# Kernel tuning notes

Measured on AMD Instinct MI355X. Metric: run time of the kernel, lower is better.

## Reference

```python
import jax, jax.numpy as jnp
import numpy as np

EMBED = 1024
HEAD = 64


def setup_inputs() -> dict:
    key = jax.random.key(0)
    kx, kq, kk, kv = jax.random.split(key, 4)
    x = jax.random.normal(kx, (8, 2048, EMBED), dtype=jnp.float32)
    s = EMBED ** -0.5  # init scale for weights
    Wq = jax.random.normal(kq, (EMBED, HEAD), dtype=jnp.float32) * s
    Wk = jax.random.normal(kk, (EMBED, HEAD), dtype=jnp.float32) * s
    Wv = jax.random.normal(kv, (EMBED, HEAD), dtype=jnp.float32) * s
    return {"x": x, "Wq": Wq, "Wk": Wk, "Wv": Wv}


def reference(x, Wq, Wk, Wv):
    # x: [B, T, C]; single-head causal attention, scale = C**-0.5 (embed dim, as in source)
    B, T, C = x.shape
    q = jnp.einsum('btc,ch->bth', x, Wq)
    k = jnp.einsum('btc,ch->bth', x, Wk)
    v = jnp.einsum('btc,ch->bth', x, Wv)
    w = jnp.einsum('bqh,bkh->bqk', q, k) * (C ** -0.5)  # [B, T, T]
    causal = jnp.tril(jnp.ones((T, T), dtype=bool))
    w = jnp.where(causal, w, -jnp.inf)
    w = jax.nn.softmax(w, axis=-1)
    # dropout = 0.0 (eval-mode reference) -> identity
    return jnp.einsum('bqk,bkh->bqh', w, v)  # [B, T, head]
```

## Files before the change

kernel.cpp:

```cpp
#include <hip/hip_runtime.h>
#include <stdint.h>

typedef unsigned short u16;
typedef __attribute__((ext_vector_type(8))) short short8;
typedef __attribute__((ext_vector_type(4))) float f32x4;
typedef __attribute__((ext_vector_type(16))) float f32x16;

#define B_ 8
#define T_ 2048
#define C_ 1024
#define D_ 64
#define PSC 0.04508422f

__device__ inline uint32_t pack2(float lo, float hi) {
  uint32_t r;
  asm("v_cvt_pk_bf16_f32 %0, %1, %2" : "=v"(r) : "v"(lo), "v"(hi));
  return r;
}
__device__ inline u16 f2bf(float f) {
  uint32_t r;
  asm("v_cvt_pk_bf16_f32 %0, %1, %2" : "=v"(r) : "v"(f), "v"(f));
  return (u16)r;
}

__global__ __launch_bounds__(256) void wt_kernel(const float* __restrict__ Wq,
                                                 const float* __restrict__ Wk,
                                                 const float* __restrict__ Wv,
                                                 u16* __restrict__ wfrag) {
  const int mi = blockIdx.x >> 4;
  const int k0 = (blockIdx.x & 15) * 64;
  const float* W = (mi == 0) ? Wq : ((mi == 1) ? Wk : Wv);
  const float sc = (mi == 0) ? PSC : 1.0f;
  __shared__ u16 tr[64 * 68];

  const int t = threadIdx.x;
  {
    const int n = t & 63, kr0 = (t >> 6) * 16;
#pragma unroll
    for (int j = 0; j < 16; ++j)
      tr[n * 68 + kr0 + j] = f2bf(W[(size_t)(k0 + kr0 + j) * 64 + n] * sc);
  }
  __syncthreads();
  {
    const int n = t >> 2, q16 = (t & 3) * 16;
    const int n16g = mi * 4 + (n >> 4);
#pragma unroll
    for (int h = 0; h < 2; ++h) {
      const int kr = q16 + h * 8;
      const int kchunk = (k0 + kr) >> 5;
      const int lane = (n & 15) + 16 * ((kr >> 3) & 3);
      uint32_t pk[4];
#pragma unroll
      for (int jj = 0; jj < 4; ++jj)
        pk[jj] = (uint32_t)tr[n * 68 + kr + 2 * jj] | ((uint32_t)tr[n * 68 + kr + 2 * jj + 1] << 16);
      *(uint4*)&wfrag[(((size_t)n16g * 32 + kchunk) * 64 + lane) * 8] = *(uint4*)&pk[0];
    }
  }
}

__global__ __launch_bounds__(512, 1) void qkv_kernel(const float* __restrict__ x,
                                                     const u16* __restrict__ wfrag,
                                                     u16* __restrict__ qfr,
                                                     u16* __restrict__ kfr,
                                                     u16* __restrict__ vfr) {
  __shared__ __align__(16) u16 xl[2][64 * 64];

  const int tid = threadIdx.x;
  const int w = tid >> 6, l = tid & 63;
  const int lo16 = l & 15, hi4 = l >> 4;
  const int wh = w & 1, ng = w >> 1;
  const int m0 = blockIdx.x * 64;

  const int xrow = tid >> 3;
  const int xc8 = tid & 7;
  const float* xs0 = x + (size_t)(m0 + xrow) * C_ + xc8 * 8;
  u16* xdst0 = &xl[0][xrow * 64 + ((xc8 ^ (xrow & 7)) << 3)];
  u16* xdst1 = &xl[1][xrow * 64 + ((xc8 ^ (xrow & 7)) << 3)];

  f32x4 acc[2][3];
#pragma unroll
  for (int rf = 0; rf < 2; ++rf)
#pragma unroll
    for (int j = 0; j < 3; ++j) acc[rf][j] = {0.f, 0.f, 0.f, 0.f};

  const u16* wbase = wfrag + (size_t)(ng * 3) * 32 * 512 + l * 8;
  short8 wA[6], wB[6];
  float4 xr1a, xr1b, xr2a, xr2b;

#define LOADW(DST, KT)                                                        \
  _Pragma("unroll")                                                           \
  for (int i = 0; i < 6; ++i)                                                 \
    DST[i] = *(const short8*)(wbase + ((i >> 1) * 32 + (KT) * 2 + (i & 1)) * 512);

#define PACKX(A0, A1, DST)                                                    \
  { uint32_t p[4] = {pack2(A0.x, A0.y), pack2(A0.z, A0.w),                    \
                     pack2(A1.x, A1.y), pack2(A1.z, A1.w)};                   \
    *(uint4*)DST = *(uint4*)&p[0]; }

#define MFMA6(XR, WC)                                                         \
  _Pragma("unroll")                                                           \
  for (int k32 = 0; k32 < 2; ++k32) {                                         \
    const int ac = k32 * 4 + hi4;                                             \
    _Pragma("unroll")                                                         \
    for (int rf = 0; rf < 2; ++rf) {                                          \
      const int arow = wh * 32 + rf * 16 + lo16;                              \
      short8 a = *(const short8*)&XR[arow * 64 + ((ac ^ (arow & 7)) << 3)];   \
      _Pragma("unroll")                                                       \
      for (int j = 0; j < 3; ++j)                                             \
        acc[rf][j] = __builtin_amdgcn_mfma_f32_16x16x32_bf16(a, WC[j * 2 + k32], acc[rf][j], 0, 0, 0); \
    }                                                                         \
  }

  {
    float4 f0 = *(const float4*)(xs0 + 0);
    float4 f1 = *(const float4*)(xs0 + 4);
    PACKX(f0, f1, xdst0)
    xr1a = *(const float4*)(xs0 + 64);
    xr1b = *(const float4*)(xs0 + 68);
    LOADW(wA, 0)
  }
  __syncthreads();

#pragma unroll 1
  for (int kt = 0; kt < 14; kt += 2) {
    xr2a = *(const float4*)(xs0 + (kt + 2) * 64);
    xr2b = *(const float4*)(xs0 + (kt + 2) * 64 + 4);
    LOADW(wB, kt + 1)
    MFMA6(xl[0], wA)
    PACKX(xr1a, xr1b, xdst1)
    __syncthreads();
    xr1a = *(const float4*)(xs0 + (kt + 3) * 64);
    xr1b = *(const float4*)(xs0 + (kt + 3) * 64 + 4);
    LOADW(wA, kt + 2)
    MFMA6(xl[1], wB)
    PACKX(xr2a, xr2b, xdst0)
    __syncthreads();
  }
  LOADW(wB, 15)
  MFMA6(xl[0], wA)
  PACKX(xr1a, xr1b, xdst1)
  __syncthreads();
  MFMA6(xl[1], wB)
#undef LOADW
#undef PACKX
#undef MFMA6

  const int bb = m0 >> 11;
  const int tok_b = m0 & 2047;
#pragma unroll
  for (int rf = 0; rf < 2; ++rf) {
    const int row0 = wh * 32 + rf * 16 + hi4 * 4;
    const int tok0 = tok_b + row0;
    const int tt = tok0 >> 6;
    const int t32 = tok0 >> 5;
#pragma unroll
    for (int j = 0; j < 3; ++j) {
      const int cb = ng * 48 + j * 16;
      const int mt = cb >> 6;
      const int col = (cb & 63) + lo16;
      if (mt == 0) {
        const int cs = col >> 4;
        const int lane0 = (tok0 & 31) + 32 * ((col >> 3) & 1);
        u16* qp = qfr + ((((size_t)bb * 64 + t32) * 4 + cs) * 64 + lane0) * 8 + (col & 7);
#pragma unroll
        for (int r = 0; r < 4; ++r) qp[(size_t)r * 8] = f2bf(acc[rf][j][r]);
      } else if (mt == 1) {
        const int h = (tok0 >> 5) & 1;
        const int cs = col >> 4;
        const int lane0 = (tok0 & 31) + 32 * ((col >> 3) & 1);
        u16* kp = kfr + (((((size_t)bb * 32 + tt) * 2 + h) * 4 + cs) * 64 + lane0) * 8 + (col & 7);
#pragma unroll
        for (int r = 0; r < 4; ++r) kp[(size_t)r * 8] = f2bf(acc[rf][j][r]);
      } else {
        const int ks = (tok0 >> 4) & 3;
        const int hi = (tok0 >> 3) & 1;
        const int jj = tok0 & 7;
        const int lane = (col & 31) + 32 * hi;
        const int df = col >> 5;
        uint2 st = {pack2(acc[rf][j][0], acc[rf][j][1]), pack2(acc[rf][j][2], acc[rf][j][3])};
        *(uint2*)&vfr[((((((size_t)bb * 32 + tt) * 4 + ks) * 2 + df) * 64 + lane) * 8 + jj)] = st;
      }
    }
  }
}

__global__ __launch_bounds__(256, 2) void attn_kernel(const u16* __restrict__ qfr,
                                                      const u16* __restrict__ kfr,
                                                      const u16* __restrict__ vfr,
                                                      float* __restrict__ out) {
  __shared__ float o_lds[4][32][68];
  __shared__ float l_lds[4][64];

  const int tid = threadIdx.x;
  const int w = tid >> 6, l = tid & 63;
  const int l31 = l & 31, hi1 = l >> 5;
  const int b = blockIdx.x;
  const int y = blockIdx.y;
  const int qt = (y < 32) ? (63 - 2 * y) : (2 * (y - 32));
  const int qbase = qt * 32;
  const int boff = b * T_;
  const int NT = (qt + 2) >> 1;

  short8 qf[4];
  {
    const u16* qp = qfr + (size_t)(b * 64 + qt) * 4 * 512 + l * 8;
#pragma unroll
    for (int cs = 0; cs < 4; ++cs) qf[cs] = *(const short8*)(qp + cs * 512);
  }

  const u16* kfb = kfr + (size_t)b * 32 * 4096 + l * 8;
  const u16* vfb = vfr + (size_t)b * 32 * 4096 + l * 8;

  f32x16 O0, O1;
#pragma unroll
  for (int r = 0; r < 16; ++r) { O0[r] = 0.f; O1[r] = 0.f; }
  float lsum = 0.f;

  short8 kf[2][4];
#define LOADK(T) { const u16* kp = kfb + (size_t)(T) * 4096; \
  _Pragma("unroll") for (int h2 = 0; h2 < 2; ++h2) \
  _Pragma("unroll") for (int cs = 0; cs < 4; ++cs) \
    kf[h2][cs] = *(const short8*)(kp + (h2 * 4 + cs) * 512); }

  if (w < NT) LOADK(w);

  union { uint32_t u[4]; short8 v; } pu;
  short8 pa[4];

#pragma unroll 1
  for (int t = w; t < NT; t += 4) {
    const int k0 = t * 64;

    short8 vf[4][2];
    {
      const u16* vp = vfb + (size_t)t * 4096;
#pragma unroll
      for (int ks = 0; ks < 4; ++ks)
#pragma unroll
        for (int df = 0; df < 2; ++df)
          vf[ks][df] = *(const short8*)(vp + (ks * 2 + df) * 512);
    }

    f32x16 s0, s1, s0b, s1b;
#pragma unroll
    for (int r = 0; r < 16; ++r) { s0[r] = 0.f; s1[r] = 0.f; s0b[r] = 0.f; s1b[r] = 0.f; }
    __builtin_amdgcn_s_setprio(1);
#pragma unroll
    for (int cs = 0; cs < 2; ++cs) {
      s0 = __builtin_amdgcn_mfma_f32_32x32x16_bf16(kf[0][cs], qf[cs], s0, 0, 0, 0);
      s1 = __builtin_amdgcn_mfma_f32_32x32x16_bf16(kf[1][cs], qf[cs], s1, 0, 0, 0);
      s0b = __builtin_amdgcn_mfma_f32_32x32x16_bf16(kf[0][cs + 2], qf[cs + 2], s0b, 0, 0, 0);
      s1b = __builtin_amdgcn_mfma_f32_32x32x16_bf16(kf[1][cs + 2], qf[cs + 2], s1b, 0, 0, 0);
    }
    __builtin_amdgcn_s_setprio(0);
#pragma unroll
    for (int r = 0; r < 16; ++r) { s0[r] += s0b[r]; s1[r] += s1b[r]; }

    if (t + 4 < NT) LOADK(t + 4);

    if (k0 + 63 > qbase) {
#pragma unroll
      for (int r = 0; r < 16; ++r) {
        const int kr = (r & 3) + 8 * (r >> 2) + 4 * hi1;
        if (k0 + kr > qbase + l31) s0[r] = -1e30f;
        if (k0 + 32 + kr > qbase + l31) s1[r] = -1e30f;
      }
    }

    float p0[16], p1[16];
    float ts[4] = {0.f, 0.f, 0.f, 0.f};
#pragma unroll
    for (int r = 0; r < 16; ++r) {
      p0[r] = exp2f(s0[r]);
      p1[r] = exp2f(s1[r]);
      ts[r & 3] += p0[r] + p1[r];
    }
    lsum += (ts[0] + ts[1]) + (ts[2] + ts[3]);

#define REDIST(KS, ARR) { \
    const int s8 = ((KS) & 1) * 8; \
    uint32_t c0a = pack2(ARR[s8 + 0], ARR[s8 + 1]); \
    uint32_t c0b = pack2(ARR[s8 + 2], ARR[s8 + 3]); \
    uint32_t c1a = pack2(ARR[s8 + 4], ARR[s8 + 5]); \
    uint32_t c1b = pack2(ARR[s8 + 6], ARR[s8 + 7]); \
    uint32_t fa = hi1 ? c0a : c1a; \
    uint32_t fb = hi1 ? c0b : c1b; \
    uint32_t ga = __shfl_xor(fa, 32); \
    uint32_t gb = __shfl_xor(fb, 32); \
    pu.u[0] = hi1 ? ga : c0a; \
    pu.u[1] = hi1 ? gb : c0b; \
    pu.u[2] = hi1 ? c1a : ga; \
    pu.u[3] = hi1 ? c1b : gb; \
    pa[KS] = pu.v; }
    REDIST(0, p0)
    REDIST(1, p0)
    REDIST(2, p1)
    REDIST(3, p1)
#undef REDIST

    __builtin_amdgcn_s_setprio(1);
#pragma unroll
    for (int ks = 0; ks < 4; ++ks) {
      O0 = __builtin_amdgcn_mfma_f32_32x32x16_bf16(pa[ks], vf[ks][0], O0, 0, 0, 0);
      O1 = __builtin_amdgcn_mfma_f32_32x32x16_bf16(pa[ks], vf[ks][1], O1, 0, 0, 0);
    }
    __builtin_amdgcn_s_setprio(0);
  }
#undef LOADK

#pragma unroll
  for (int r = 0; r < 16; ++r) {
    const int qr = (r & 3) + 8 * (r >> 2) + 4 * hi1;
    o_lds[w][qr][l31] = O0[r];
    o_lds[w][qr][32 + l31] = O1[r];
  }
  l_lds[w][l] = lsum;
  __syncthreads();

  {
    const int q = tid >> 3;
    const int d8 = (tid & 7) * 8;
    float lacc = 0.f;
    float oacc[8] = {0.f, 0.f, 0.f, 0.f, 0.f, 0.f, 0.f, 0.f};
#pragma unroll
    for (int s = 0; s < 4; ++s) {
      lacc += l_lds[s][q] + l_lds[s][q + 32];
#pragma unroll
      for (int j = 0; j < 8; ++j) oacc[j] += o_lds[s][q][d8 + j];
    }
    const float inv = 1.f / lacc;
    float4 r0 = {oacc[0] * inv, oacc[1] * inv, oacc[2] * inv, oacc[3] * inv};
    float4 r1 = {oacc[4] * inv, oacc[5] * inv, oacc[6] * inv, oacc[7] * inv};
    float* op = out + (size_t)(boff + qbase + q) * 64 + d8;
    *(float4*)(op + 0) = r0;
    *(float4*)(op + 4) = r1;
  }
}

extern "C" void kernel_launch(void* const* d_in, const int* in_sizes, int n_in,
                              void* d_out, int out_size, void* d_ws, size_t ws_size,
                              hipStream_t stream) {
  const float* x  = (const float*)d_in[0];
  const float* Wq = (const float*)d_in[1];
  const float* Wk = (const float*)d_in[2];
  const float* Wv = (const float*)d_in[3];
  float* out = (float*)d_out;

  u16* ws    = (u16*)d_ws;
  u16* wfrag = ws;
  u16* qfr   = ws + 196608;
  u16* kfr   = qfr + 1048576;
  u16* vfr   = kfr + 1048576;

  wt_kernel<<<dim3(48), dim3(256), 0, stream>>>(Wq, Wk, Wv, wfrag);
  qkv_kernel<<<dim3(256), dim3(512), 0, stream>>>(x, wfrag, qfr, kfr, vfr);
  attn_kernel<<<dim3(8, 64), dim3(256), 0, stream>>>(qfr, kfr, vfr, out);
}
```

Baseline: 35.75 us.

## Process two K-tiles per barrier in QKV projection using four LDS buffers

The QKV projection kernel now keeps four x tiles in shared memory instead of two. Each loop iteration consumes two k-tiles and stages the next two, so there is one __syncthreads per pair of tiles rather than one per tile. The intent is to halve barrier count and give loads more time in flight before they are used. In exchange the kernel uses twice the LDS for x and needs more live registers for the prefetched x and weights.

```diff
diff --git a/kernel.cpp b/kernel.cpp
--- a/kernel.cpp
+++ b/kernel.cpp
@@ -63,7 +63,7 @@
                                                      u16* __restrict__ qfr,
                                                      u16* __restrict__ kfr,
                                                      u16* __restrict__ vfr) {
-  __shared__ __align__(16) u16 xl[2][64 * 64];
+  __shared__ __align__(16) u16 xl[4][64 * 64];
 
   const int tid = threadIdx.x;
   const int w = tid >> 6, l = tid & 63;
@@ -74,8 +74,8 @@
   const int xrow = tid >> 3;
   const int xc8 = tid & 7;
   const float* xs0 = x + (size_t)(m0 + xrow) * C_ + xc8 * 8;
-  u16* xdst0 = &xl[0][xrow * 64 + ((xc8 ^ (xrow & 7)) << 3)];
-  u16* xdst1 = &xl[1][xrow * 64 + ((xc8 ^ (xrow & 7)) << 3)];
+  u16* const xflat = &xl[0][0];
+  const int xoff = xrow * 64 + ((xc8 ^ (xrow & 7)) << 3);
 
   f32x4 acc[2][3];
 #pragma unroll
@@ -85,26 +85,26 @@
 
   const u16* wbase = wfrag + (size_t)(ng * 3) * 32 * 512 + l * 8;
   short8 wA[6], wB[6];
-  float4 xr1a, xr1b, xr2a, xr2b;
+  float4 xr2a, xr2b, xr3a, xr3b;
 
 #define LOADW(DST, KT)                                                        \
   _Pragma("unroll")                                                           \
   for (int i = 0; i < 6; ++i)                                                 \
     DST[i] = *(const short8*)(wbase + ((i >> 1) * 32 + (KT) * 2 + (i & 1)) * 512);
 
-#define PACKX(A0, A1, DST)                                                    \
+#define PACKX(A0, A1, BOFF)                                                   \
   { uint32_t p[4] = {pack2(A0.x, A0.y), pack2(A0.z, A0.w),                    \
                      pack2(A1.x, A1.y), pack2(A1.z, A1.w)};                   \
-    *(uint4*)DST = *(uint4*)&p[0]; }
-
-#define MFMA6(XR, WC)                                                         \
+    *(uint4*)(xflat + (BOFF) + xoff) = *(uint4*)&p[0]; }
+
+#define MFMA6(BOFF, WC)                                                       \
   _Pragma("unroll")                                                           \
   for (int k32 = 0; k32 < 2; ++k32) {                                         \
     const int ac = k32 * 4 + hi4;                                             \
     _Pragma("unroll")                                                         \
     for (int rf = 0; rf < 2; ++rf) {                                          \
       const int arow = wh * 32 + rf * 16 + lo16;                              \
-      short8 a = *(const short8*)&XR[arow * 64 + ((ac ^ (arow & 7)) << 3)];   \
+      short8 a = *(const short8*)(xflat + (BOFF) + arow * 64 + ((ac ^ (arow & 7)) << 3)); \
       _Pragma("unroll")                                                       \
       for (int j = 0; j < 3; ++j)                                             \
         acc[rf][j] = __builtin_amdgcn_mfma_f32_16x16x32_bf16(a, WC[j * 2 + k32], acc[rf][j], 0, 0, 0); \
@@ -114,33 +114,34 @@
   {
     float4 f0 = *(const float4*)(xs0 + 0);
     float4 f1 = *(const float4*)(xs0 + 4);
-    PACKX(f0, f1, xdst0)
-    xr1a = *(const float4*)(xs0 + 64);
-    xr1b = *(const float4*)(xs0 + 68);
+    PACKX(f0, f1, 0)
+    float4 f2 = *(const float4*)(xs0 + 64);
+    float4 f3 = *(const float4*)(xs0 + 68);
+    PACKX(f2, f3, 4096)
     LOADW(wA, 0)
+    LOADW(wB, 1)
   }
   __syncthreads();
 
 #pragma unroll 1
   for (int kt = 0; kt < 14; kt += 2) {
+    const int ib = kt & 3;
+    const int rb = ib << 12;
+    const int wb = (ib ^ 2) << 12;
     xr2a = *(const float4*)(xs0 + (kt + 2) * 64);
     xr2b = *(const float4*)(xs0 + (kt + 2) * 64 + 4);
-    LOADW(wB, kt + 1)
-    MFMA6(xl[0], wA)
-    PACKX(xr1a, xr1b, xdst1)
+    xr3a = *(const float4*)(xs0 + (kt + 3) * 64);
+    xr3b = *(const float4*)(xs0 + (kt + 3) * 64 + 4);
+    MFMA6(rb, wA)
+    LOADW(wA, kt + 2)
+    MFMA6(rb + 4096, wB)
+    LOADW(wB, kt + 3)
+    PACKX(xr2a, xr2b, wb)
+    PACKX(xr3a, xr3b, wb + 4096)
     __syncthreads();
-    xr1a = *(const float4*)(xs0 + (kt + 3) * 64);
-    xr1b = *(const float4*)(xs0 + (kt + 3) * 64 + 4);
-    LOADW(wA, kt + 2)
-    MFMA6(xl[1], wB)
-    PACKX(xr2a, xr2b, xdst0)
-    __syncthreads();
-  }
-  LOADW(wB, 15)
-  MFMA6(xl[0], wA)
-  PACKX(xr1a, xr1b, xdst1)
-  __syncthreads();
-  MFMA6(xl[1], wB)
+  }
+  MFMA6(2 * 4096, wA)
+  MFMA6(3 * 4096, wB)
 #undef LOADW
 #undef PACKX
 #undef MFMA6
```

After: 39.93 us. 1.12x slower.

## Split attention head dimension across two blocks to double grid parallelism

Applied to the files above, without the earlier changes.

Each attention block now computes only half of the 64-wide output head dimension, selected by blockIdx.y, and the grid grows to 128 in y. QK^T and softmax are recomputed redundantly in both halves, while each block does half the PV MFMAs and loads half the V fragments. The aim is more blocks and waves in flight and shorter per-block latency, traded against duplicated score computation and K traffic.

```diff
diff --git a/kernel.cpp b/kernel.cpp
--- a/kernel.cpp
+++ b/kernel.cpp
@@ -188,7 +188,7 @@
                                                       const u16* __restrict__ kfr,
                                                       const u16* __restrict__ vfr,
                                                       float* __restrict__ out) {
-  __shared__ float o_lds[4][32][68];
+  __shared__ float o_lds[4][32][36];
   __shared__ float l_lds[4][64];
 
   const int tid = threadIdx.x;
@@ -196,7 +196,9 @@
   const int l31 = l & 31, hi1 = l >> 5;
   const int b = blockIdx.x;
   const int y = blockIdx.y;
-  const int qt = (y < 32) ? (63 - 2 * y) : (2 * (y - 32));
+  const int dh = y >> 6;
+  const int yy = y & 63;
+  const int qt = (yy < 32) ? (63 - 2 * yy) : (2 * (yy - 32));
   const int qbase = qt * 32;
   const int boff = b * T_;
   const int NT = (qt + 2) >> 1;
@@ -209,11 +211,11 @@
   }
 
   const u16* kfb = kfr + (size_t)b * 32 * 4096 + l * 8;
-  const u16* vfb = vfr + (size_t)b * 32 * 4096 + l * 8;
-
-  f32x16 O0, O1;
-#pragma unroll
-  for (int r = 0; r < 16; ++r) { O0[r] = 0.f; O1[r] = 0.f; }
+  const u16* vfb = vfr + (size_t)b * 32 * 4096 + l * 8 + dh * 512;
+
+  f32x16 O0;
+#pragma unroll
+  for (int r = 0; r < 16; ++r) O0[r] = 0.f;
   float lsum = 0.f;
 
   short8 kf[2][4];
@@ -231,14 +233,12 @@
   for (int t = w; t < NT; t += 4) {
     const int k0 = t * 64;
 
-    short8 vf[4][2];
+    short8 vf[4];
     {
       const u16* vp = vfb + (size_t)t * 4096;
 #pragma unroll
       for (int ks = 0; ks < 4; ++ks)
-#pragma unroll
-        for (int df = 0; df < 2; ++df)
-          vf[ks][df] = *(const short8*)(vp + (ks * 2 + df) * 512);
+        vf[ks] = *(const short8*)(vp + ks * 1024);
     }
 
     f32x16 s0, s1, s0b, s1b;
@@ -300,10 +300,8 @@
 
     __builtin_amdgcn_s_setprio(1);
 #pragma unroll
-    for (int ks = 0; ks < 4; ++ks) {
-      O0 = __builtin_amdgcn_mfma_f32_32x32x16_bf16(pa[ks], vf[ks][0], O0, 0, 0, 0);
-      O1 = __builtin_amdgcn_mfma_f32_32x32x16_bf16(pa[ks], vf[ks][1], O1, 0, 0, 0);
-    }
+    for (int ks = 0; ks < 4; ++ks)
+      O0 = __builtin_amdgcn_mfma_f32_32x32x16_bf16(pa[ks], vf[ks], O0, 0, 0, 0);
     __builtin_amdgcn_s_setprio(0);
   }
 #undef LOADK
@@ -312,28 +310,24 @@
   for (int r = 0; r < 16; ++r) {
     const int qr = (r & 3) + 8 * (r >> 2) + 4 * hi1;
     o_lds[w][qr][l31] = O0[r];
-    o_lds[w][qr][32 + l31] = O1[r];
   }
   l_lds[w][l] = lsum;
   __syncthreads();
 
   {
     const int q = tid >> 3;
-    const int d8 = (tid & 7) * 8;
+    const int dc = (tid & 7) * 4;
     float lacc = 0.f;
-    float oacc[8] = {0.f, 0.f, 0.f, 0.f, 0.f, 0.f, 0.f, 0.f};
+    float oacc[4] = {0.f, 0.f, 0.f, 0.f};
 #pragma unroll
     for (int s = 0; s < 4; ++s) {
       lacc += l_lds[s][q] + l_lds[s][q + 32];
 #pragma unroll
-      for (int j = 0; j < 8; ++j) oacc[j] += o_lds[s][q][d8 + j];
+      for (int j = 0; j < 4; ++j) oacc[j] += o_lds[s][q][dc + j];
     }
     const float inv = 1.f / lacc;
     float4 r0 = {oacc[0] * inv, oacc[1] * inv, oacc[2] * inv, oacc[3] * inv};
-    float4 r1 = {oacc[4] * inv, oacc[5] * inv, oacc[6] * inv, oacc[7] * inv};
-    float* op = out + (size_t)(boff + qbase + q) * 64 + d8;
-    *(float4*)(op + 0) = r0;
-    *(float4*)(op + 4) = r1;
+    *(float4*)&out[(size_t)(boff + qbase + q) * 64 + dh * 32 + dc] = r0;
   }
 }
 
@@ -354,5 +348,5 @@
 
   wt_kernel<<<dim3(48), dim3(256), 0, stream>>>(Wq, Wk, Wv, wfrag);
   qkv_kernel<<<dim3(256), dim3(512), 0, stream>>>(x, wfrag, qfr, kfr, vfr);
-  attn_kernel<<<dim3(8, 64), dim3(256), 0, stream>>>(qfr, kfr, vfr, out);
-}
+  attn_kernel<<<dim3(8, 128), dim3(256), 0, stream>>>(qfr, kfr, vfr, out);
+}
```

Result: slower. 44.13 us (+23.4%).
